# Kernel tuning notes

Measured on AMD Instinct MI355X. Metric: run time of the kernel, lower is better.

Reference implementation:

```python
import jax, jax.numpy as jnp
import numpy as np

B, N, K = 16, 100000, 8


def compute_laplacian(x, nbs_idxs, nbs_weights):
    # x: [B, N, 3]; nbs_idxs: [N, K]; nbs_weights: [N, K]
    gathered = x[:, nbs_idxs]  # [B, N, K, 3]
    return x + (gathered * nbs_weights[None, :, :, None]).sum(axis=2)


def setup_inputs() -> dict:
    key = jax.random.key(0)
    k1, k2, k3, k4 = jax.random.split(key, 4)
    geom = jax.random.normal(k1, (B, N, 3), dtype=jnp.float32)
    geom_template_posed = jax.random.normal(k2, (B, N, 3), dtype=jnp.float32)
    nbs_idxs = jax.random.randint(k3, (N, K), 0, N, dtype=jnp.int32)
    nbs_weights = jax.random.normal(k4, (N, K), dtype=jnp.float32)
    return {
        "geom": geom,
        "geom_template_posed": geom_template_posed,
        "nbs_idxs": nbs_idxs,
        "nbs_weights": nbs_weights,
    }


def reference(geom, geom_template_posed, nbs_idxs, nbs_weights):
    l_preds = compute_laplacian(geom, nbs_idxs, nbs_weights)
    # targets side is detached in the original (stop_gradient)
    l_targets = compute_laplacian(jax.lax.stop_gradient(geom_template_posed), nbs_idxs, nbs_weights)
    diff = l_preds - l_targets
    return jnp.mean(diff * diff)
```

## Files before the change

### kernel.cpp

```cpp
#include <hip/hip_runtime.h>

#define BB 16
#define NN 100000
#define KK 8
#define BLOCK 256

#define ROW_U4 4
#define DT_BYTES ((size_t)NN * 64)
#define GRID1 ((NN + 63) / 64)
#define GRID2 (NN * 8 / BLOCK)
#define SCALE (1.0f / ((float)BB * NN * 3))

typedef float f32x2 __attribute__((ext_vector_type(2)));

__device__ __forceinline__ unsigned pk_fp8x4(float a, float b, float c, float d) {
    int v = __builtin_amdgcn_cvt_pk_fp8_f32(a, b, 0, false);
    v     = __builtin_amdgcn_cvt_pk_fp8_f32(c, d, v, true);
    return (unsigned)v;
}

__device__ __forceinline__ void fma16(float* a, uint4 u, float wv) {
    f32x2 p;
    p = __builtin_amdgcn_cvt_pk_f32_fp8((int)u.x, false); a[0]  += wv * p.x; a[1]  += wv * p.y;
    p = __builtin_amdgcn_cvt_pk_f32_fp8((int)u.x, true ); a[2]  += wv * p.x; a[3]  += wv * p.y;
    p = __builtin_amdgcn_cvt_pk_f32_fp8((int)u.y, false); a[4]  += wv * p.x; a[5]  += wv * p.y;
    p = __builtin_amdgcn_cvt_pk_f32_fp8((int)u.y, true ); a[6]  += wv * p.x; a[7]  += wv * p.y;
    p = __builtin_amdgcn_cvt_pk_f32_fp8((int)u.z, false); a[8]  += wv * p.x; a[9]  += wv * p.y;
    p = __builtin_amdgcn_cvt_pk_f32_fp8((int)u.z, true ); a[10] += wv * p.x; a[11] += wv * p.y;
    p = __builtin_amdgcn_cvt_pk_f32_fp8((int)u.w, false); a[12] += wv * p.x; a[13] += wv * p.y;
    p = __builtin_amdgcn_cvt_pk_f32_fp8((int)u.w, true ); a[14] += wv * p.x; a[15] += wv * p.y;
}

__global__ __launch_bounds__(BLOCK) void diff_transpose_fp8_kernel(
    const float4* __restrict__ geom4,
    const float4* __restrict__ gtp4,
    uint4*        __restrict__ dT4)
{
    __shared__ float tile[64][49];
    int tid = threadIdx.x;
    int b = tid >> 4;
    int q = tid & 15;
    int nbase = blockIdx.x * 64;
    int n0 = nbase + q * 4;

    if (n0 < NN) {
        int fi = (b * (NN * 3) + n0 * 3) >> 2;
        float4 g0 = geom4[fi], g1 = geom4[fi + 1], g2 = geom4[fi + 2];
        float4 t0 = gtp4[fi],  t1 = gtp4[fi + 1],  t2 = gtp4[fi + 2];
        float d[12] = {g0.x - t0.x, g0.y - t0.y, g0.z - t0.z, g0.w - t0.w,
                       g1.x - t1.x, g1.y - t1.y, g1.z - t1.z, g1.w - t1.w,
                       g2.x - t2.x, g2.y - t2.y, g2.z - t2.z, g2.w - t2.w};
        #pragma unroll
        for (int e = 0; e < 12; ++e)
            tile[q * 4 + e / 3][b * 3 + e % 3] = d[e];
    }
    __syncthreads();

    {
        int r = tid >> 2, m = tid & 3;
        int n = nbase + r;
        if (n < NN) {
            uint4 o;
            if (m < 3) {
                const float* row = &tile[r][m * 16];
                o.x = pk_fp8x4(row[0],  row[1],  row[2],  row[3]);
                o.y = pk_fp8x4(row[4],  row[5],  row[6],  row[7]);
                o.z = pk_fp8x4(row[8],  row[9],  row[10], row[11]);
                o.w = pk_fp8x4(row[12], row[13], row[14], row[15]);
            } else {
                o.x = o.y = o.z = o.w = 0u;
            }
            dT4[n * ROW_U4 + m] = o;
        }
    }
}

__global__ __launch_bounds__(BLOCK) void lap_gather_kernel(
    const uint4* __restrict__ dv,
    const int*   __restrict__ idx,
    const float* __restrict__ w,
    float*       __restrict__ partial)
{
    int t = blockIdx.x * BLOCK + threadIdx.x;
    int n = t >> 3;
    int h = (t >> 2) & 1;
    int s = t & 3;

    float a[16];
    #pragma unroll
    for (int i = 0; i < 16; ++i) a[i] = 0.0f;

    const int4*   ip = reinterpret_cast<const int4*>(idx + (size_t)n * KK);
    const float4* wp = reinterpret_cast<const float4*>(w + (size_t)n * KK);
    int4   iv = ip[h];
    float4 wv = wp[h];
    int   js[4] = {iv.x, iv.y, iv.z, iv.w};
    float wk[4] = {wv.x, wv.y, wv.z, wv.w};

    #pragma unroll
    for (int k = 0; k < 4; ++k)
        fma16(a, dv[js[k] * ROW_U4 + s], wk[k]);

    if (h == 0)
        fma16(a, dv[n * ROW_U4 + s], 1.0f);

    float ssq = 0.0f;
    #pragma unroll
    for (int i = 0; i < 16; ++i) ssq += a[i] * a[i];

    #pragma unroll
    for (int off = 32; off > 0; off >>= 1)
        ssq += __shfl_down(ssq, off, 64);

    __shared__ float wsum[BLOCK / 64];
    int lane = threadIdx.x & 63;
    int wid  = threadIdx.x >> 6;
    if (lane == 0) wsum[wid] = ssq;
    __syncthreads();

    if (threadIdx.x == 0)
        partial[blockIdx.x] = wsum[0] + wsum[1] + wsum[2] + wsum[3];
}

__global__ __launch_bounds__(BLOCK) void final_reduce_kernel(
    const float* __restrict__ partial,
    float*       __restrict__ out)
{
    float s = 0.0f;
    for (int i = threadIdx.x; i < GRID2; i += BLOCK)
        s += partial[i];

    #pragma unroll
    for (int off = 32; off > 0; off >>= 1)
        s += __shfl_down(s, off, 64);

    __shared__ float wsum[BLOCK / 64];
    int lane = threadIdx.x & 63;
    int wid  = threadIdx.x >> 6;
    if (lane == 0) wsum[wid] = s;
    __syncthreads();

    if (threadIdx.x == 0)
        out[0] = (wsum[0] + wsum[1] + wsum[2] + wsum[3]) * SCALE;
}

extern "C" void kernel_launch(void* const* d_in, const int* in_sizes, int n_in,
                              void* d_out, int out_size, void* d_ws, size_t ws_size,
                              hipStream_t stream) {
    const float* geom = (const float*)d_in[0];
    const float* gtp  = (const float*)d_in[1];
    const int*   idx  = (const int*)d_in[2];
    const float* w    = (const float*)d_in[3];
    float* out = (float*)d_out;

    uint4* dT4     = (uint4*)d_ws;
    float* partial = (float*)((char*)d_ws + DT_BYTES);

    diff_transpose_fp8_kernel<<<GRID1, BLOCK, 0, stream>>>(
        (const float4*)geom, (const float4*)gtp, dT4);
    lap_gather_kernel<<<GRID2, BLOCK, 0, stream>>>(dT4, idx, w, partial);
    final_reduce_kernel<<<1, BLOCK, 0, stream>>>(partial, out);
}
```

Baseline: 28.52 us.

## Split fp8 diff table into two 32-byte planes and regroup gather threads

The fp8 difference table moves from one 64-byte row per vertex (48 used bytes plus padding) to two 32-byte planes. Each plane holds half the batches, so each gathered neighbour row is a single 32-byte segment. The gather kernel now gives each thread two neighbours and both planes instead of four neighbours on one 16-byte slice, with the goal of cutting wasted bandwidth on random gathers. The final reduce also runs with 1024 threads instead of 256. Each 32-byte plane still carries 8 bytes of zero padding, and the zero words are still fed through the unpack-and-FMA code.

```diff
diff --git a/kernel.cpp b/kernel.cpp
--- a/kernel.cpp
+++ b/kernel.cpp
@@ -5,8 +5,8 @@
 #define KK 8
 #define BLOCK 256
 
-#define ROW_U4 4
-#define DT_BYTES ((size_t)NN * 64)
+#define PLANE_U4 2
+#define PLANE_BYTES ((size_t)NN * 32)
 #define GRID1 ((NN + 63) / 64)
 #define GRID2 (NN * 8 / BLOCK)
 #define SCALE (1.0f / ((float)BB * NN * 3))
@@ -34,7 +34,8 @@
 __global__ __launch_bounds__(BLOCK) void diff_transpose_fp8_kernel(
     const float4* __restrict__ geom4,
     const float4* __restrict__ gtp4,
-    uint4*        __restrict__ dT4)
+    uint4*        __restrict__ dA4,
+    uint4*        __restrict__ dB4)
 {
     __shared__ float tile[64][49];
     int tid = threadIdx.x;
@@ -60,51 +61,68 @@
         int r = tid >> 2, m = tid & 3;
         int n = nbase + r;
         if (n < NN) {
+            const float* row = &tile[r][0];
             uint4 o;
-            if (m < 3) {
-                const float* row = &tile[r][m * 16];
+            if (m == 0) {
                 o.x = pk_fp8x4(row[0],  row[1],  row[2],  row[3]);
                 o.y = pk_fp8x4(row[4],  row[5],  row[6],  row[7]);
                 o.z = pk_fp8x4(row[8],  row[9],  row[10], row[11]);
                 o.w = pk_fp8x4(row[12], row[13], row[14], row[15]);
+                dA4[n * PLANE_U4 + 0] = o;
+            } else if (m == 1) {
+                o.x = pk_fp8x4(row[16], row[17], row[18], row[19]);
+                o.y = pk_fp8x4(row[20], row[21], row[22], row[23]);
+                o.z = 0u; o.w = 0u;
+                dA4[n * PLANE_U4 + 1] = o;
+            } else if (m == 2) {
+                o.x = pk_fp8x4(row[24], row[25], row[26], row[27]);
+                o.y = pk_fp8x4(row[28], row[29], row[30], row[31]);
+                o.z = pk_fp8x4(row[32], row[33], row[34], row[35]);
+                o.w = pk_fp8x4(row[36], row[37], row[38], row[39]);
+                dB4[n * PLANE_U4 + 0] = o;
             } else {
-                o.x = o.y = o.z = o.w = 0u;
+                o.x = pk_fp8x4(row[40], row[41], row[42], row[43]);
+                o.y = pk_fp8x4(row[44], row[45], row[46], row[47]);
+                o.z = 0u; o.w = 0u;
+                dB4[n * PLANE_U4 + 1] = o;
             }
-            dT4[n * ROW_U4 + m] = o;
         }
     }
 }
 
 __global__ __launch_bounds__(BLOCK) void lap_gather_kernel(
-    const uint4* __restrict__ dv,
+    const uint4* __restrict__ dA,
+    const uint4* __restrict__ dB,
     const int*   __restrict__ idx,
     const float* __restrict__ w,
     float*       __restrict__ partial)
 {
     int t = blockIdx.x * BLOCK + threadIdx.x;
     int n = t >> 3;
-    int h = (t >> 2) & 1;
-    int s = t & 3;
+    int p = (t >> 1) & 3;
+    int s = t & 1;
 
+    int2  iv = reinterpret_cast<const int2*>(idx + (size_t)n * KK)[p];
+    f32x2 wv = reinterpret_cast<const f32x2*>(w + (size_t)n * KK)[p];
+
+    float ssq = 0.0f;
     float a[16];
+
     #pragma unroll
     for (int i = 0; i < 16; ++i) a[i] = 0.0f;
-
-    const int4*   ip = reinterpret_cast<const int4*>(idx + (size_t)n * KK);
-    const float4* wp = reinterpret_cast<const float4*>(w + (size_t)n * KK);
-    int4   iv = ip[h];
-    float4 wv = wp[h];
-    int   js[4] = {iv.x, iv.y, iv.z, iv.w};
-    float wk[4] = {wv.x, wv.y, wv.z, wv.w};
+    fma16(a, dA[iv.x * PLANE_U4 + s], wv.x);
+    fma16(a, dA[iv.y * PLANE_U4 + s], wv.y);
+    if (p == 0)
+        fma16(a, dA[n * PLANE_U4 + s], 1.0f);
+    #pragma unroll
+    for (int i = 0; i < 16; ++i) ssq += a[i] * a[i];
 
     #pragma unroll
-    for (int k = 0; k < 4; ++k)
-        fma16(a, dv[js[k] * ROW_U4 + s], wk[k]);
-
-    if (h == 0)
-        fma16(a, dv[n * ROW_U4 + s], 1.0f);
-
-    float ssq = 0.0f;
+    for (int i = 0; i < 16; ++i) a[i] = 0.0f;
+    fma16(a, dB[iv.x * PLANE_U4 + s], wv.x);
+    fma16(a, dB[iv.y * PLANE_U4 + s], wv.y);
+    if (p == 0)
+        fma16(a, dB[n * PLANE_U4 + s], 1.0f);
     #pragma unroll
     for (int i = 0; i < 16; ++i) ssq += a[i] * a[i];
 
@@ -122,26 +140,30 @@
         partial[blockIdx.x] = wsum[0] + wsum[1] + wsum[2] + wsum[3];
 }
 
-__global__ __launch_bounds__(BLOCK) void final_reduce_kernel(
+__global__ __launch_bounds__(1024) void final_reduce_kernel(
     const float* __restrict__ partial,
     float*       __restrict__ out)
 {
     float s = 0.0f;
-    for (int i = threadIdx.x; i < GRID2; i += BLOCK)
+    for (int i = threadIdx.x; i < GRID2; i += 1024)
         s += partial[i];
 
     #pragma unroll
     for (int off = 32; off > 0; off >>= 1)
         s += __shfl_down(s, off, 64);
 
-    __shared__ float wsum[BLOCK / 64];
+    __shared__ float wsum[1024 / 64];
     int lane = threadIdx.x & 63;
     int wid  = threadIdx.x >> 6;
     if (lane == 0) wsum[wid] = s;
     __syncthreads();
 
-    if (threadIdx.x == 0)
-        out[0] = (wsum[0] + wsum[1] + wsum[2] + wsum[3]) * SCALE;
+    if (threadIdx.x == 0) {
+        float sum = 0.0f;
+        #pragma unroll
+        for (int i = 0; i < 1024 / 64; ++i) sum += wsum[i];
+        out[0] = sum * SCALE;
+    }
 }
 
 extern "C" void kernel_launch(void* const* d_in, const int* in_sizes, int n_in,
@@ -153,11 +175,12 @@
     const float* w    = (const float*)d_in[3];
     float* out = (float*)d_out;
 
-    uint4* dT4     = (uint4*)d_ws;
-    float* partial = (float*)((char*)d_ws + DT_BYTES);
+    uint4* dA4     = (uint4*)d_ws;
+    uint4* dB4     = (uint4*)((char*)d_ws + PLANE_BYTES);
+    float* partial = (float*)((char*)d_ws + 2 * PLANE_BYTES);
 
     diff_transpose_fp8_kernel<<<GRID1, BLOCK, 0, stream>>>(
-        (const float4*)geom, (const float4*)gtp, dT4);
-    lap_gather_kernel<<<GRID2, BLOCK, 0, stream>>>(dT4, idx, w, partial);
-    final_reduce_kernel<<<1, BLOCK, 0, stream>>>(partial, out);
+        (const float4*)geom, (const float4*)gtp, dA4, dB4);
+    lap_gather_kernel<<<GRID2, BLOCK, 0, stream>>>(dA4, dB4, idx, w, partial);
+    final_reduce_kernel<<<1, 1024, 0, stream>>>(partial, out);
 }
```

After: 31.57 us. 10.7% more time.
